# Kernel tuning notes

Measured on AMD Instinct MI355X. Metric: run time of the kernel, lower is better.

The kernel has to match this reference:

```python
import jax, jax.numpy as jnp
import numpy as np

B, C, D, S = 1024, 128, 16, 4        # nodes, channels (mul), irrep feature dim (0e+1o+2e+3o), species
K3, K2, K1 = 23, 5, 2                # generalized-CG path counts for correlation 3/2/1
OUT_DIMS = (1, 3)                    # target irreps 0e (dim 1) and 1o (dim 3)


def setup_inputs() -> dict:
    key = jax.random.key(0)
    ks = jax.random.split(key, 12)
    f = lambda k, s: jax.random.normal(k, s, dtype=jnp.float32)
    U_SCALE = 0.05  # keep corr-3 products numerically moderate (stand-in CG basis)
    return {
        "node_feats": f(ks[0], (B, C, D)),
        "u3_0": f(ks[1], (1, D, D, D, K3)) * U_SCALE,
        "u3_1": f(ks[2], (3, D, D, D, K3)) * U_SCALE,
        "u2_0": f(ks[3], (1, D, D, K2)) * U_SCALE,
        "u2_1": f(ks[4], (3, D, D, K2)) * U_SCALE,
        "u1_0": f(ks[5], (1, D, K1)) * U_SCALE,
        "u1_1": f(ks[6], (3, D, K1)) * U_SCALE,
        "w3": f(ks[7], (2, S, K3, C)) / np.sqrt(K3),
        "w2": f(ks[8], (2, S, K2, C)) / np.sqrt(K2),
        "w1": f(ks[9], (2, S, K1, C)) / np.sqrt(K1),
        "w_lin": f(ks[10], (2, C, C)),
        "node_species": jax.random.randint(ks[11], (B,), 0, S, dtype=jnp.int32),
    }


def _sym_contract(x, sp, u3, u2, u1, w3, w2, w1):
    """MACE symmetric contraction for one output irrep.
    x: (B,C,D); u3: (do,D,D,D,K3); u2: (do,D,D,K2); u1: (do,D,K1);
    w*: (S,K*,C) per-species path weights. Returns (B,C,do)."""
    onehot = jax.nn.one_hot(sp, S, dtype=x.dtype)        # (B,S)
    # corr-3 main term: fold species weights into the basis once (small: S*C*do*D^3)
    uw3 = jnp.einsum('oijlk,ekc->ecoijl', u3, w3)        # (S,C,do,D,D,D)
    do = u3.shape[0]
    out = jnp.zeros((x.shape[0], x.shape[1], do, D, D), x.dtype)
    for e in range(S):  # fixed small species loop (irregular per-species access)
        out = out + onehot[:, e][:, None, None, None, None] * \
            jnp.einsum('coijl,bcl->bcoij', uw3[e], x)
    # corr-2: add weighted basis, contract one feature axis
    c2 = jnp.einsum('oijk,bkc->bcoij', u2, w2[sp]) + out
    out = jnp.einsum('bcoij,bcj->bcoi', c2, x)
    # corr-1
    c1 = jnp.einsum('oik,bkc->bcoi', u1, w1[sp]) + out
    return jnp.einsum('bcoi,bci->bco', c1, x)            # (B,C,do)


def reference(node_feats, u3_0, u3_1, u2_0, u2_1, u1_0, u1_1, w3, w2, w1, w_lin, node_species):
    y0 = _sym_contract(node_feats, node_species, u3_0, u2_0, u1_0, w3[0], w2[0], w1[0])
    y1 = _sym_contract(node_feats, node_species, u3_1, u2_1, u1_1, w3[1], w2[1], w1[1])
    # equivariant Linear(target_irreps): mix multiplicity channels per irrep, 1/sqrt(fan_in)
    scale = 1.0 / jnp.sqrt(jnp.asarray(C, node_feats.dtype))
    z0 = jnp.einsum('bco,cn->bno', y0, w_lin[0]) * scale  # (B,C,1)
    z1 = jnp.einsum('bco,cn->bno', y1, w_lin[1]) * scale  # (B,C,3)
    # axis_to_mul flattening: (B, C*1 + C*3)
    return jnp.concatenate([z0.reshape(B, C * 1), z1.reshape(B, C * 3)], axis=1)
```

## Files before the change

### kernel.cpp

```cpp
#include <hip/hip_runtime.h>
#include <hip/hip_bf16.h>

#define SS 4
#define CC 128
#define WELEM 18432
#define NK3 23
#define NK2 5
#define NK1 2
#define DLP 72

typedef unsigned int uint;
typedef unsigned short ushort;
typedef __attribute__((ext_vector_type(8))) short bf16x8;
typedef __attribute__((ext_vector_type(4))) float f32x4;

__device__ __forceinline__ float bflo(uint u){ return __uint_as_float(u << 16); }
__device__ __forceinline__ float bfhi(uint u){ return __uint_as_float(u & 0xffff0000u); }
__device__ __forceinline__ ushort f2bf(float f) {
  uint u = __float_as_uint(f);
  return (ushort)((u + 0x7fffu + ((u >> 16) & 1u)) >> 16);
}
__device__ __forceinline__ uint pk2(float a, float b) {
  __hip_bfloat162 h = __float22bfloat162_rn(make_float2(a, b));
  return *(uint*)&h;
}

__global__ __launch_bounds__(256) void pre_kernel(
    const float* __restrict__ u3_0, const float* __restrict__ u3_1,
    const float* __restrict__ w3,
    const float* __restrict__ u2_0, const float* __restrict__ u2_1,
    const float* __restrict__ u1_0, const float* __restrict__ u1_1,
    const float* __restrict__ w2,  const float* __restrict__ w1,
    const int* __restrict__ sp, ushort* __restrict__ W,
    int* __restrict__ sorted, int* __restrict__ seg) {
  __shared__ float smem[5888 + NK3 * 64];
  int bx = blockIdx.x;
  int tid = threadIdx.x;

  if (bx < 512) {
    float* u3s = smem;
    float* w3s = smem + 5888;
    int ch = bx & 1, i = (bx >> 1) & 15, o = (bx >> 5) & 3, s = bx >> 7;
    int g = (o > 0) ? 1 : 0, og = g ? (o - 1) : 0;
    const float* u3 = g ? u3_1 : u3_0;

    const float4* u3p = (const float4*)(u3 + (size_t)(og * 16 + i) * 5888);
    for (int d = tid; d < 1472; d += 256) {
      float4 v = u3p[d];
      u3s[4 * d] = v.x; u3s[4 * d + 1] = v.y; u3s[4 * d + 2] = v.z; u3s[4 * d + 3] = v.w;
    }
    for (int t = tid; t < NK3 * 64; t += 256) {
      int k = t >> 6, cp = t & 63;
      w3s[t] = w3[((size_t)(g * SS + s) * NK3 + k) * CC + ch * 64 + cp];
    }
    __syncthreads();

    float acc[64];
    #pragma unroll
    for (int q = 0; q < 64; q++) acc[q] = 0.f;
    int jl = tid;
    for (int k = 0; k < NK3; k++) {
      float u3v = u3s[jl * NK3 + k];
      const float4* wp = (const float4*)&w3s[k * 64];
      #pragma unroll
      for (int cq = 0; cq < 16; cq++) {
        float4 wv = wp[cq];
        acc[cq * 4 + 0] = fmaf(u3v, wv.x, acc[cq * 4 + 0]);
        acc[cq * 4 + 1] = fmaf(u3v, wv.y, acc[cq * 4 + 1]);
        acc[cq * 4 + 2] = fmaf(u3v, wv.z, acc[cq * 4 + 2]);
        acc[cq * 4 + 3] = fmaf(u3v, wv.w, acc[cq * 4 + 3]);
      }
    }
    int n = o * 16 + i;
    #pragma unroll
    for (int cp = 0; cp < 64; cp++) {
      W[(size_t)(s * CC + ch * 64 + cp) * WELEM + n * 256 + jl] = f2bf(acc[cp]);
    }
  } else if (bx < 1024) {
    int b2 = bx - 512;
    int s = b2 >> 7, c = b2 & 127;
    int n = tid >> 2, lq = tid & 3;
    int o = n >> 4, i = n & 15;
    int g = (o > 0) ? 1 : 0, og = g ? (o - 1) : 0;
    const float* u2 = g ? u2_1 : u2_0;
    const float* u1 = g ? u1_1 : u1_0;

    float vals[8];
    #pragma unroll
    for (int t = 0; t < 8; t++) {
      int k = 256 + lq * 8 + t;
      float v = 0.f;
      if (k < 272) {
        int j = k - 256;
        #pragma unroll
        for (int k2 = 0; k2 < NK2; k2++)
          v = fmaf(u2[((size_t)(og * 16 + i) * 16 + j) * NK2 + k2],
                   w2[((size_t)(g * SS + s) * NK2 + k2) * CC + c], v);
      } else if (k == 272) {
        #pragma unroll
        for (int k2 = 0; k2 < NK1; k2++)
          v = fmaf(u1[(size_t)(og * 16 + i) * NK1 + k2],
                   w1[((size_t)(g * SS + s) * NK1 + k2) * CC + c], v);
      }
      vals[t] = v;
    }
    uint4 pk;
    pk.x = pk2(vals[0], vals[1]); pk.y = pk2(vals[2], vals[3]);
    pk.z = pk2(vals[4], vals[5]); pk.w = pk2(vals[6], vals[7]);
    size_t base = (size_t)(s * CC + c) * WELEM;
    size_t off = 16384 + ((size_t)o * 64 + lq * 16 + i) * 8;
    *(uint4*)(W + base + off) = pk;
  } else {
    __shared__ int cnt[SS];
    __shared__ int basep[SS + 1];
    if (tid < SS) cnt[tid] = 0;
    __syncthreads();
    int mysp[4], mypos[4];
    #pragma unroll
    for (int q = 0; q < 4; q++) {
      int node = q * 256 + tid;
      int s = sp[node];
      mysp[q] = s;
      mypos[q] = atomicAdd(&cnt[s], 1);
    }
    __syncthreads();
    if (tid == 0) {
      basep[0] = 0;
      for (int q = 0; q < SS; q++) basep[q + 1] = basep[q] + cnt[q];
      for (int q = 0; q <= SS; q++) seg[q] = basep[q];
    }
    __syncthreads();
    #pragma unroll
    for (int q = 0; q < 4; q++)
      sorted[basep[mysp[q]] + mypos[q]] = q * 256 + tid;
  }
}

__global__ __launch_bounds__(256, 2) void corr_kernel(
    const float* __restrict__ xg, const ushort* __restrict__ Wg,
    const int* __restrict__ sorted, const int* __restrict__ seg,
    float* __restrict__ y) {
  __shared__ uint4 Wl4[2304];
  __shared__ __align__(16) float xl[2][4][16][20];
  __shared__ __align__(16) ushort Dl[4 * 16 * DLP];
  int bx = blockIdx.x;
  int s = bx >> 7, c = bx & 127;
  int tid = threadIdx.x;
  int w = tid >> 6, lane = tid & 63;
  int lq = lane >> 4, ln = lane & 15;

  const uint4* wg = (const uint4*)(Wg + (size_t)(s * CC + c) * WELEM);

  for (int d = tid; d < 2048; d += 256) {
    int n = d >> 5, j = d & 31;
    int kt = j >> 2, lqj = j & 3;
    Wl4[(kt * 4 + (n >> 4)) * 64 + ((lqj * 16 + (n & 15)) ^ kt)] = wg[d];
  }
  Wl4[2048 + tid] = wg[2048 + tid];

  int s0 = seg[s], s1 = seg[s + 1];
  int nslab = (s1 - s0 + 63) >> 6;
  int npair = (nslab + 1) >> 1;

  int sv0 = 0, sv1 = 0;
  if (nslab > 0) {
    int r0 = s0 + w * 16 + ln;
    sv0 = sorted[min(r0, s1 - 1)];
    float4 v0 = *((const float4*)(xg + ((size_t)sv0 * CC + c) * 16) + lq);
    *(float4*)(&xl[0][w][ln][lq * 4]) = v0;
    int r1 = s0 + 64 + w * 16 + ln;
    sv1 = sorted[min(r1, s1 - 1)];
    float4 v1 = *((const float4*)(xg + ((size_t)sv1 * CC + c) * 16) + lq);
    *(float4*)(&xl[1][w][ln][lq * 4]) = v1;
  }
  __syncthreads();

  for (int t = 0; t < npair; t++) {
    float xvA[16], xvB[16];
    #pragma unroll
    for (int q = 0; q < 4; q++) {
      float4 va = *(const float4*)(&xl[0][w][ln][q * 4]);
      xvA[q * 4] = va.x; xvA[q * 4 + 1] = va.y; xvA[q * 4 + 2] = va.z; xvA[q * 4 + 3] = va.w;
      float4 vb = *(const float4*)(&xl[1][w][ln][q * 4]);
      xvB[q * 4] = vb.x; xvB[q * 4 + 1] = vb.y; xvB[q * 4 + 2] = vb.z; xvB[q * 4 + 3] = vb.w;
    }
    int svA = sv0, svB = sv1;
    int rowA = s0 + (2 * t) * 64 + w * 16 + ln;
    int rowB = rowA + 64;
    float4 xc0 = make_float4(0.f, 0.f, 0.f, 0.f);
    float4 xc1 = make_float4(0.f, 0.f, 0.f, 0.f);
    bool pf = (t + 1 < npair);
    if (pf) {
      int r0 = s0 + (2 * t + 2) * 64 + w * 16 + ln;
      sv0 = sorted[min(r0, s1 - 1)];
      xc0 = *((const float4*)(xg + ((size_t)sv0 * CC + c) * 16) + lq);
      int r1 = min(r0 + 64, s1 - 1);
      sv1 = sorted[r1];
      xc1 = *((const float4*)(xg + ((size_t)sv1 * CC + c) * 16) + lq);
    }

    float xs8A[8], xs8B[8];
    #pragma unroll
    for (int q = 0; q < 8; q++) {
      xs8A[q] = (lq & 1) ? xvA[8 + q] : xvA[q];
      xs8B[q] = (lq & 1) ? xvB[8 + q] : xvB[q];
    }

    f32x4 accA[4], accB[4];
    #pragma unroll
    for (int nt = 0; nt < 4; nt++) {
      accA[nt] = (f32x4){0.f, 0.f, 0.f, 0.f};
      accB[nt] = (f32x4){0.f, 0.f, 0.f, 0.f};
    }

    #pragma unroll
    for (int kt = 0; kt < 9; kt++) {
      uint4 avA, avB;
      if (kt < 8) {
        float xjA = (lq & 2) ? xvA[kt * 2 + 1] : xvA[kt * 2];
        avA.x = pk2(xjA * xs8A[0], xjA * xs8A[1]);
        avA.y = pk2(xjA * xs8A[2], xjA * xs8A[3]);
        avA.z = pk2(xjA * xs8A[4], xjA * xs8A[5]);
        avA.w = pk2(xjA * xs8A[6], xjA * xs8A[7]);
        float xjB = (lq & 2) ? xvB[kt * 2 + 1] : xvB[kt * 2];
        avB.x = pk2(xjB * xs8B[0], xjB * xs8B[1]);
        avB.y = pk2(xjB * xs8B[2], xjB * xs8B[3]);
        avB.z = pk2(xjB * xs8B[4], xjB * xs8B[5]);
        avB.w = pk2(xjB * xs8B[6], xjB * xs8B[7]);
      } else {
        avA.x = pk2(xs8A[0], xs8A[1]); avA.y = pk2(xs8A[2], xs8A[3]);
        avA.z = pk2(xs8A[4], xs8A[5]); avA.w = pk2(xs8A[6], xs8A[7]);
        avB.x = pk2(xs8B[0], xs8B[1]); avB.y = pk2(xs8B[2], xs8B[3]);
        avB.z = pk2(xs8B[4], xs8B[5]); avB.w = pk2(xs8B[6], xs8B[7]);
        if (lq == 2) { avA = make_uint4(0x3f80u, 0u, 0u, 0u); avB = avA; }
        if (lq == 3) { avA = make_uint4(0u, 0u, 0u, 0u); avB = avA; }
      }
      bf16x8 aA = *(bf16x8*)&avA;
      bf16x8 aB = *(bf16x8*)&avB;
      #pragma unroll
      for (int nt = 0; nt < 4; nt++) {
        uint4 bv;
        if (kt < 8) bv = Wl4[(kt * 4 + nt) * 64 + (lane ^ kt)];
        else        bv = Wl4[2048 + nt * 64 + lane];
        bf16x8 b = *(bf16x8*)&bv;
        accA[nt] = __builtin_amdgcn_mfma_f32_16x16x32_bf16(aA, b, accA[nt], 0, 0, 0);
        accB[nt] = __builtin_amdgcn_mfma_f32_16x16x32_bf16(aB, b, accB[nt], 0, 0, 0);
      }
    }

    #pragma unroll
    for (int nt = 0; nt < 4; nt++)
      #pragma unroll
      for (int r = 0; r < 4; r++)
        Dl[(w * 16 + lq * 4 + r) * DLP + nt * 16 + ln] = f2bf(accA[nt][r]);
    {
      const uint4* dp = (const uint4*)&Dl[(w * 16 + ln) * DLP + lq * 16];
      uint4 d0 = dp[0], d1 = dp[1];
      float r = 0.f;
      r = fmaf(bflo(d0.x), xvA[0],  r); r = fmaf(bfhi(d0.x), xvA[1],  r);
      r = fmaf(bflo(d0.y), xvA[2],  r); r = fmaf(bfhi(d0.y), xvA[3],  r);
      r = fmaf(bflo(d0.z), xvA[4],  r); r = fmaf(bfhi(d0.z), xvA[5],  r);
      r = fmaf(bflo(d0.w), xvA[6],  r); r = fmaf(bfhi(d0.w), xvA[7],  r);
      r = fmaf(bflo(d1.x), xvA[8],  r); r = fmaf(bfhi(d1.x), xvA[9],  r);
      r = fmaf(bflo(d1.y), xvA[10], r); r = fmaf(bfhi(d1.y), xvA[11], r);
      r = fmaf(bflo(d1.z), xvA[12], r); r = fmaf(bfhi(d1.z), xvA[13], r);
      r = fmaf(bflo(d1.w), xvA[14], r); r = fmaf(bfhi(d1.w), xvA[15], r);
      if (rowA < s1)
        y[((size_t)svA * CC + c) * 4 + lq] = r;
    }
    #pragma unroll
    for (int nt = 0; nt < 4; nt++)
      #pragma unroll
      for (int r = 0; r < 4; r++)
        Dl[(w * 16 + lq * 4 + r) * DLP + nt * 16 + ln] = f2bf(accB[nt][r]);
    {
      const uint4* dp = (const uint4*)&Dl[(w * 16 + ln) * DLP + lq * 16];
      uint4 d0 = dp[0], d1 = dp[1];
      float r = 0.f;
      r = fmaf(bflo(d0.x), xvB[0],  r); r = fmaf(bfhi(d0.x), xvB[1],  r);
      r = fmaf(bflo(d0.y), xvB[2],  r); r = fmaf(bfhi(d0.y), xvB[3],  r);
      r = fmaf(bflo(d0.z), xvB[4],  r); r = fmaf(bfhi(d0.z), xvB[5],  r);
      r = fmaf(bflo(d0.w), xvB[6],  r); r = fmaf(bfhi(d0.w), xvB[7],  r);
      r = fmaf(bflo(d1.x), xvB[8],  r); r = fmaf(bfhi(d1.x), xvB[9],  r);
      r = fmaf(bflo(d1.y), xvB[10], r); r = fmaf(bfhi(d1.y), xvB[11], r);
      r = fmaf(bflo(d1.z), xvB[12], r); r = fmaf(bfhi(d1.z), xvB[13], r);
      r = fmaf(bflo(d1.w), xvB[14], r); r = fmaf(bfhi(d1.w), xvB[15], r);
      if (rowB < s1)
        y[((size_t)svB * CC + c) * 4 + lq] = r;
    }

    if (pf) {
      *(float4*)(&xl[0][w][ln][lq * 4]) = xc0;
      *(float4*)(&xl[1][w][ln][lq * 4]) = xc1;
    }
  }
}

__global__ __launch_bounds__(128) void lin_kernel(
    const float* __restrict__ y, const float* __restrict__ w_lin,
    float* __restrict__ out) {
  int b = blockIdx.x;
  int n = threadIdx.x;
  const float4* yb4 = (const float4*)(y + (size_t)b * 512);
  float a0 = 0.f, a1 = 0.f, a2 = 0.f, a3 = 0.f;
  #pragma unroll 8
  for (int cc = 0; cc < CC; cc++) {
    float4 yv = yb4[cc];
    float wl0 = w_lin[(size_t)cc * CC + n];
    float wl1 = w_lin[16384 + (size_t)cc * CC + n];
    a0 = fmaf(yv.x, wl0, a0);
    a1 = fmaf(yv.y, wl1, a1);
    a2 = fmaf(yv.z, wl1, a2);
    a3 = fmaf(yv.w, wl1, a3);
  }
  const float scale = 0.08838834764831845f;
  out[(size_t)b * 512 + n] = a0 * scale;
  out[(size_t)b * 512 + 128 + (size_t)n * 3 + 0] = a1 * scale;
  out[(size_t)b * 512 + 128 + (size_t)n * 3 + 1] = a2 * scale;
  out[(size_t)b * 512 + 128 + (size_t)n * 3 + 2] = a3 * scale;
}

extern "C" void kernel_launch(void* const* d_in, const int* in_sizes, int n_in,
                              void* d_out, int out_size, void* d_ws, size_t ws_size,
                              hipStream_t stream) {
  const float* node_feats = (const float*)d_in[0];
  const float* u3_0 = (const float*)d_in[1];
  const float* u3_1 = (const float*)d_in[2];
  const float* u2_0 = (const float*)d_in[3];
  const float* u2_1 = (const float*)d_in[4];
  const float* u1_0 = (const float*)d_in[5];
  const float* u1_1 = (const float*)d_in[6];
  const float* w3   = (const float*)d_in[7];
  const float* w2   = (const float*)d_in[8];
  const float* w1   = (const float*)d_in[9];
  const float* wlin = (const float*)d_in[10];
  const int* species = (const int*)d_in[11];
  float* out = (float*)d_out;

  char* ws = (char*)d_ws;
  ushort* W  = (ushort*)ws;
  float* yb  = (float*)(ws + 18874368);
  int* sorted = (int*)(ws + 20971520);
  int* seg    = (int*)(ws + 20975616);

  pre_kernel<<<1025, 256, 0, stream>>>(u3_0, u3_1, w3, u2_0, u2_1, u1_0, u1_1,
                                       w2, w1, species, W, sorted, seg);
  corr_kernel<<<512, 256, 0, stream>>>(node_feats, W, sorted, seg, yb);
  lin_kernel<<<1024, 128, 0, stream>>>(yb, wlin, out);
}
```

Baseline: 129.7 us.

## Split node slabs across two blocks and read weights from global memory

Result: slower. 222.3 us (+71.4%).

```diff
diff --git a/kernel.cpp b/kernel.cpp
--- a/kernel.cpp
+++ b/kernel.cpp
@@ -3,6 +3,7 @@
 
 #define SS 4
 #define CC 128
+#define KROW 288
 #define WELEM 18432
 #define NK3 23
 #define NK2 5
@@ -74,7 +75,7 @@
     int n = o * 16 + i;
     #pragma unroll
     for (int cp = 0; cp < 64; cp++) {
-      W[(size_t)(s * CC + ch * 64 + cp) * WELEM + n * 256 + jl] = f2bf(acc[cp]);
+      W[(size_t)(s * CC + ch * 64 + cp) * WELEM + n * KROW + jl] = f2bf(acc[cp]);
     }
   } else if (bx < 1024) {
     int b2 = bx - 512;
@@ -107,9 +108,7 @@
     uint4 pk;
     pk.x = pk2(vals[0], vals[1]); pk.y = pk2(vals[2], vals[3]);
     pk.z = pk2(vals[4], vals[5]); pk.w = pk2(vals[6], vals[7]);
-    size_t base = (size_t)(s * CC + c) * WELEM;
-    size_t off = 16384 + ((size_t)o * 64 + lq * 16 + i) * 8;
-    *(uint4*)(W + base + off) = pk;
+    *(uint4*)(W + (size_t)(s * CC + c) * WELEM + n * KROW + 256 + lq * 8) = pk;
   } else {
     __shared__ int cnt[SS];
     __shared__ int basep[SS + 1];
@@ -136,46 +135,37 @@
   }
 }
 
-__global__ __launch_bounds__(256, 2) void corr_kernel(
+__global__ __launch_bounds__(256, 3) void corr_kernel(
     const float* __restrict__ xg, const ushort* __restrict__ Wg,
     const int* __restrict__ sorted, const int* __restrict__ seg,
     float* __restrict__ y) {
-  __shared__ uint4 Wl4[2304];
   __shared__ __align__(16) float xl[2][4][16][20];
   __shared__ __align__(16) ushort Dl[4 * 16 * DLP];
   int bx = blockIdx.x;
-  int s = bx >> 7, c = bx & 127;
+  int h = bx >> 9, s = (bx >> 7) & 3, c = bx & 127;
   int tid = threadIdx.x;
   int w = tid >> 6, lane = tid & 63;
   int lq = lane >> 4, ln = lane & 15;
 
-  const uint4* wg = (const uint4*)(Wg + (size_t)(s * CC + c) * WELEM);
-
-  for (int d = tid; d < 2048; d += 256) {
-    int n = d >> 5, j = d & 31;
-    int kt = j >> 2, lqj = j & 3;
-    Wl4[(kt * 4 + (n >> 4)) * 64 + ((lqj * 16 + (n & 15)) ^ kt)] = wg[d];
-  }
-  Wl4[2048 + tid] = wg[2048 + tid];
+  const ushort* wgu = Wg + (size_t)(s * CC + c) * WELEM + ln * KROW + lq * 8;
 
   int s0 = seg[s], s1 = seg[s + 1];
   int nslab = (s1 - s0 + 63) >> 6;
   int npair = (nslab + 1) >> 1;
 
   int sv0 = 0, sv1 = 0;
-  if (nslab > 0) {
-    int r0 = s0 + w * 16 + ln;
+  if (h < npair) {
+    int r0 = s0 + (2 * h) * 64 + w * 16 + ln;
     sv0 = sorted[min(r0, s1 - 1)];
     float4 v0 = *((const float4*)(xg + ((size_t)sv0 * CC + c) * 16) + lq);
     *(float4*)(&xl[0][w][ln][lq * 4]) = v0;
-    int r1 = s0 + 64 + w * 16 + ln;
-    sv1 = sorted[min(r1, s1 - 1)];
+    int r1 = min(r0 + 64, s1 - 1);
+    sv1 = sorted[r1];
     float4 v1 = *((const float4*)(xg + ((size_t)sv1 * CC + c) * 16) + lq);
     *(float4*)(&xl[1][w][ln][lq * 4]) = v1;
   }
-  __syncthreads();
-
-  for (int t = 0; t < npair; t++) {
+
+  for (int t = h; t < npair; t += 2) {
     float xvA[16], xvB[16];
     #pragma unroll
     for (int q = 0; q < 4; q++) {
@@ -189,9 +179,9 @@
     int rowB = rowA + 64;
     float4 xc0 = make_float4(0.f, 0.f, 0.f, 0.f);
     float4 xc1 = make_float4(0.f, 0.f, 0.f, 0.f);
-    bool pf = (t + 1 < npair);
+    bool pf = (t + 2 < npair);
     if (pf) {
-      int r0 = s0 + (2 * t + 2) * 64 + w * 16 + ln;
+      int r0 = s0 + (2 * t + 4) * 64 + w * 16 + ln;
       sv0 = sorted[min(r0, s1 - 1)];
       xc0 = *((const float4*)(xg + ((size_t)sv0 * CC + c) * 16) + lq);
       int r1 = min(r0 + 64, s1 - 1);
@@ -239,9 +229,7 @@
       bf16x8 aB = *(bf16x8*)&avB;
       #pragma unroll
       for (int nt = 0; nt < 4; nt++) {
-        uint4 bv;
-        if (kt < 8) bv = Wl4[(kt * 4 + nt) * 64 + (lane ^ kt)];
-        else        bv = Wl4[2048 + nt * 64 + lane];
+        uint4 bv = *(const uint4*)(wgu + nt * (16 * KROW) + kt * 32);
         bf16x8 b = *(bf16x8*)&bv;
         accA[nt] = __builtin_amdgcn_mfma_f32_16x16x32_bf16(aA, b, accA[nt], 0, 0, 0);
         accB[nt] = __builtin_amdgcn_mfma_f32_16x16x32_bf16(aB, b, accB[nt], 0, 0, 0);
@@ -345,6 +333,6 @@
 
   pre_kernel<<<1025, 256, 0, stream>>>(u3_0, u3_1, w3, u2_0, u2_1, u1_0, u1_1,
                                        w2, w1, species, W, sorted, seg);
-  corr_kernel<<<512, 256, 0, stream>>>(node_feats, W, sorted, seg, yb);
+  corr_kernel<<<1024, 256, 0, stream>>>(node_feats, W, sorted, seg, yb);
   lin_kernel<<<1024, 128, 0, stream>>>(yb, wlin, out);
 }
```
